# Performance work log

Hardware: AMD Instinct MI355X
Metric: run time of the kernel (lower is better)

Reference implementation:

```python
import jax, jax.numpy as jnp
import numpy as np

E, DIM, HID, OUT = 8, 128, 512, 128
B, HH, WW = 16, 64, 64
N = HH * WW
EPS = 1e-6


def setup_inputs() -> dict:
    key = jax.random.key(0)
    ks = jax.random.split(key, 8)
    return {
        "x": jax.random.normal(ks[0], (B, N, DIM), jnp.float32),
        "H": HH,
        "W": WW,
        "wg": jax.random.normal(ks[1], (DIM, E), jnp.float32) * 0.02,
        "bg": jnp.zeros((E,), jnp.float32),
        "W1": jax.random.normal(ks[2], (E, DIM, HID), jnp.float32) * 0.02,
        "B1": jnp.zeros((E, HID), jnp.float32),
        "Wd": jax.random.normal(ks[3], (E, 3, 3, 1, HID), jnp.float32) * np.sqrt(2.0 / 9.0),
        "Bd": jnp.zeros((E, HID), jnp.float32),
        "W2": jax.random.normal(ks[4], (E, HID, OUT), jnp.float32) * 0.02,
        "B2": jnp.zeros((E, OUT), jnp.float32),
    }


def reference(x, H, W, wg, bg, W1, B1, Wd, Bd, W2, B2):
    Bb, Nn, C = x.shape
    e = wg.shape[1]
    hid = W1.shape[2]

    # ---- SwitchGate (faithful to original, including the dim-1 scatter) ----
    gate_scores = jax.nn.softmax(x @ wg + bg, axis=-1)  # (B,N,E)
    capacity = float(int(1.0 * Bb))  # capacity_factor = 1.0
    top1 = jnp.argmax(gate_scores, axis=-1)  # (B,N)
    # torch: zeros_like(gs).scatter_(1, idx, 1) -> mask[b, idx[b,n,0], 0] = 1
    mask = jnp.zeros_like(gate_scores).at[jnp.arange(Bb)[:, None], top1, 0].set(1.0)
    masked = gate_scores * mask
    denom = masked.sum(axis=0, keepdims=True) + EPS
    gate_scores = masked / denom * capacity
    gate_scores = jnp.nan_to_num(gate_scores)

    # ---- all-experts MixFFN (fc1 -> dwconv -> gelu -> fc2) ----
    h = jnp.einsum('bnd,edh->ebnh', x, W1) + B1[:, None, None, :]  # (E,B,N,hid)
    h = h.reshape(e, Bb, H, W, hid)  # NHWC per expert

    def expert_dwconv(hi, k, bb):
        y = jax.lax.conv_general_dilated(
            hi, k, window_strides=(1, 1), padding='SAME',
            dimension_numbers=('NHWC', 'HWIO', 'NHWC'),
            feature_group_count=hid)
        return y + bb

    h = jax.vmap(expert_dwconv)(h, Wd, Bd)  # (E,B,H,W,hid)
    h = jax.nn.gelu(h.reshape(e, Bb, Nn, hid), approximate=False)
    expert_out = jnp.einsum('ebnh,eho->ebno', h, W2) + B2[:, None, None, :]  # (E,B,N,O)
    expert_out = jnp.nan_to_num(expert_out)

    # weighted combine: sum_e gate[b,n,e] * expert_out[e,b,n,:]
    moe_output = jnp.einsum('bne,ebno->bno', gate_scores, expert_out)
    return moe_output
```

## Files before the change

kernel.cpp:

```cpp
#include <hip/hip_runtime.h>
#include <math.h>

#define NB   16
#define NTOK 4096
#define DIM  128
#define NE   8
#define HID  512
#define NOUT 128
#define GBLK 512


__global__ __launch_bounds__(256) void gate_kernel(
    const float4* __restrict__ x,
    const float* __restrict__ wg,
    const float* __restrict__ bg,
    float* __restrict__ s0,
    unsigned char* __restrict__ hitpart,
    float4* __restrict__ out)
{
    __shared__ float4 lw4[NE][DIM / 4];
    __shared__ float lbg[NE];
    __shared__ unsigned int lmask;

    int tid = threadIdx.x;
    {
        int e = tid >> 5, s = tid & 31, d0 = s * 4;
        float4 w;
        w.x = wg[(d0 + 0) * NE + e];
        w.y = wg[(d0 + 1) * NE + e];
        w.z = wg[(d0 + 2) * NE + e];
        w.w = wg[(d0 + 3) * NE + e];
        lw4[e][s] = w;
    }
    if (tid < NE) lbg[tid] = bg[tid];
    if (tid == 0) lmask = 0u;
    __syncthreads();

    int sub  = tid & 7;
    int tgrp = tid >> 3;

    float4 wv[NE][4];
    #pragma unroll
    for (int e = 0; e < NE; e++)
        #pragma unroll
        for (int k = 0; k < 4; k++) wv[e][k] = lw4[e][sub + 8 * k];

    #pragma unroll 2
    for (int it = 0; it < 4; it++) {
        int tok = (blockIdx.x << 7) + (it << 5) + tgrp;
        int b   = tok >> 12;
        int n   = tok & 4095;
        size_t base = (size_t)tok * 32 + sub;

        float4 zz = make_float4(0.f, 0.f, 0.f, 0.f);
        out[base]      = zz;
        out[base + 8]  = zz;
        out[base + 16] = zz;
        out[base + 24] = zz;

        float4 xv0 = x[base];
        float4 xv1 = x[base + 8];
        float4 xv2 = x[base + 16];
        float4 xv3 = x[base + 24];

        float z[NE];
        #pragma unroll
        for (int e = 0; e < NE; e++) {
            z[e] = xv0.x * wv[e][0].x + xv0.y * wv[e][0].y
                 + xv0.z * wv[e][0].z + xv0.w * wv[e][0].w
                 + xv1.x * wv[e][1].x + xv1.y * wv[e][1].y
                 + xv1.z * wv[e][1].z + xv1.w * wv[e][1].w
                 + xv2.x * wv[e][2].x + xv2.y * wv[e][2].y
                 + xv2.z * wv[e][2].z + xv2.w * wv[e][2].w
                 + xv3.x * wv[e][3].x + xv3.y * wv[e][3].y
                 + xv3.z * wv[e][3].z + xv3.w * wv[e][3].w;
        }

        #pragma unroll
        for (int off = 1; off <= 4; off <<= 1) {
            #pragma unroll
            for (int e = 0; e < NE; e++) z[e] += __shfl_xor(z[e], off);
        }

        if (sub == 0) {
            float zf[NE];
            #pragma unroll
            for (int e = 0; e < NE; e++) zf[e] = z[e] + lbg[e];

            int am = 0;
            float mz = zf[0];
            #pragma unroll
            for (int e = 1; e < NE; e++) {
                if (zf[e] > mz) { mz = zf[e]; am = e; }
            }
            atomicOr(&lmask, 1u << am);

            if (n < 8) {
                float s = 0.f;
                #pragma unroll
                for (int e = 0; e < NE; e++) s += expf(zf[e] - mz);
                s0[b * NE + n] = expf(zf[0] - mz) / s;
            }
        }
    }

    __syncthreads();
    if (tid == 0) hitpart[blockIdx.x] = (unsigned char)lmask;
}

__global__ __launch_bounds__(256) void expert_kernel(
    const float* __restrict__ x,
    const float* __restrict__ W1,
    const float* __restrict__ B1,
    const float* __restrict__ Wd,
    const float* __restrict__ Bd,
    const float* __restrict__ W2,
    const float* __restrict__ B2,
    const float* __restrict__ s0,
    const unsigned char* __restrict__ hitpart,
    float* __restrict__ out)
{
    __shared__ float4 xs4[6][32];
    __shared__ float4 redb[128][6];
    __shared__ float gls[HID];
    __shared__ float red2[256];
    __shared__ unsigned int hm[NB];
    __shared__ float gate_s;

    int b = blockIdx.x >> 3;
    int w = blockIdx.x & 7;
    int tid = threadIdx.x;

    if (tid < NB) {
        const uint4* hp = (const uint4*)hitpart;
        uint4 v0 = hp[tid * 2], v1 = hp[tid * 2 + 1];
        unsigned int m = v0.x | v0.y | v0.z | v0.w | v1.x | v1.y | v1.z | v1.w;
        m |= m >> 16; m |= m >> 8; m &= 0xffu;
        hm[tid] = m;
    }

    if (tid < 192) {
        int p = tid >> 5, dq = tid & 31;
        int row = p / 3, ci = p % 3;
        int col = w - 1 + ci;
        if (col < 0) col = 0;
        xs4[p][dq] = ((const float4*)x)[((size_t)b * NTOK + row * 64 + col) * 32 + dq];
    }
    __syncthreads();

    if (tid == 0) {
        float denom = 1e-6f, mine = 0.f;
        for (int bb = 0; bb < NB; bb++) {
            float v = ((hm[bb] >> w) & 1u) ? s0[bb * NE + w] : 0.f;
            denom += v;
            if (bb == b) mine = v;
        }
        gate_s = 16.0f * mine / denom;
    }

    int q  = tid & 127;
    int kh = tid >> 7;
    float4 acc[6];
    #pragma unroll
    for (int p = 0; p < 6; p++) acc[p] = make_float4(0.f, 0.f, 0.f, 0.f);

    const float4* W14 = (const float4*)W1;
    #pragma unroll 4
    for (int s = 0; s < 16; s++) {
        int d0 = kh * 64 + s * 4;
        float4 wv0 = W14[(size_t)(d0 + 0) * 128 + q];
        float4 wv1 = W14[(size_t)(d0 + 1) * 128 + q];
        float4 wv2 = W14[(size_t)(d0 + 2) * 128 + q];
        float4 wv3 = W14[(size_t)(d0 + 3) * 128 + q];
        #pragma unroll
        for (int p = 0; p < 6; p++) {
            float4 xv = xs4[p][kh * 16 + s];
            acc[p].x += xv.x * wv0.x + xv.y * wv1.x + xv.z * wv2.x + xv.w * wv3.x;
            acc[p].y += xv.x * wv0.y + xv.y * wv1.y + xv.z * wv2.y + xv.w * wv3.y;
            acc[p].z += xv.x * wv0.z + xv.y * wv1.z + xv.z * wv2.z + xv.w * wv3.z;
            acc[p].w += xv.x * wv0.w + xv.y * wv1.w + xv.z * wv2.w + xv.w * wv3.w;
        }
    }

    if (kh == 1) {
        #pragma unroll
        for (int p = 0; p < 6; p++) redb[q][p] = acc[p];
    }
    __syncthreads();

    if (kh == 0) {
        #pragma unroll
        for (int p = 0; p < 6; p++) {
            float4 r = redb[q][p];
            acc[p].x += r.x; acc[p].y += r.y; acc[p].z += r.z; acc[p].w += r.w;
        }
        float4 b1 = ((const float4*)B1)[q];
        float4 y  = ((const float4*)Bd)[q];
        #pragma unroll
        for (int ci = 0; ci < 3; ci++) {
            int col = w - 1 + ci;
            if (col < 0) continue;
            float4 wda = ((const float4*)Wd)[(3 + ci) * 128 + q];
            float4 wdb = ((const float4*)Wd)[(6 + ci) * 128 + q];
            float4 a0 = acc[ci];
            float4 a1 = acc[3 + ci];
            y.x += (a0.x + b1.x) * wda.x + (a1.x + b1.x) * wdb.x;
            y.y += (a0.y + b1.y) * wda.y + (a1.y + b1.y) * wdb.y;
            y.z += (a0.z + b1.z) * wda.z + (a1.z + b1.z) * wdb.z;
            y.w += (a0.w + b1.w) * wda.w + (a1.w + b1.w) * wdb.w;
        }
        const float k = 0.70710678118654752f;
        float4 g;
        g.x = 0.5f * y.x * (1.0f + erff(y.x * k));
        g.y = 0.5f * y.y * (1.0f + erff(y.y * k));
        g.z = 0.5f * y.z * (1.0f + erff(y.z * k));
        g.w = 0.5f * y.w * (1.0f + erff(y.w * k));
        ((float4*)gls)[q] = g;
    }
    __syncthreads();

    int o    = tid & 127;
    int half = tid >> 7;
    const float* wp = W2 + (size_t)(half * 256) * NOUT + o;
    const float4* gp = (const float4*)&gls[half * 256];
    float a = 0.f;
    #pragma unroll
    for (int cb = 0; cb < 256; cb += 32) {
        float wv[32];
        #pragma unroll
        for (int k2 = 0; k2 < 32; k2++) wv[k2] = wp[(size_t)(cb + k2) * NOUT];
        #pragma unroll
        for (int k2 = 0; k2 < 32; k2 += 4) {
            float4 g = gp[(cb + k2) >> 2];
            a += g.x * wv[k2] + g.y * wv[k2 + 1] + g.z * wv[k2 + 2] + g.w * wv[k2 + 3];
        }
    }
    red2[tid] = a;
    __syncthreads();
    if (tid < 128) {
        out[((size_t)b * NTOK + w) * NOUT + o] =
            (red2[tid] + red2[tid + 128] + B2[o]) * gate_s;
    }
}

extern "C" void kernel_launch(void* const* d_in, const int* in_sizes, int n_in,
                              void* d_out, int out_size, void* d_ws, size_t ws_size,
                              hipStream_t stream) {
    const float* x  = (const float*)d_in[0];
    const float* wg = (const float*)d_in[3];
    const float* bg = (const float*)d_in[4];
    const float* W1 = (const float*)d_in[5];
    const float* B1 = (const float*)d_in[6];
    const float* Wd = (const float*)d_in[7];
    const float* Bd = (const float*)d_in[8];
    const float* W2 = (const float*)d_in[9];
    const float* B2 = (const float*)d_in[10];

    float* s0              = (float*)d_ws;
    unsigned char* hitpart = (unsigned char*)d_ws + 512;

    gate_kernel<<<GBLK, 256, 0, stream>>>(
        (const float4*)x, wg, bg, s0, hitpart, (float4*)d_out);
    expert_kernel<<<NB * 8, 256, 0, stream>>>(
        x, W1, B1, Wd, Bd, W2, B2, s0, hitpart, (float*)d_out);
}
```

Before: 121.9 us.

## Fuse gate and expert kernels into one launch with global-counter sync

Merges the gating kernel and the expert kernel into a single launch. The expert blocks come first in the grid so their MLP work overlaps with the gate blocks. Before writing output, each expert block spin-waits on a global counter until all gate blocks have published their hit masks and softmax values, and a second counter resets state for the next call. It also uses nontemporal loads and stores for x and the zero-fill, and skips zeroing rows the expert blocks overwrite. This removes a kernel launch boundary, but it relies on gate blocks making progress while expert blocks spin, and that forward progress is not guaranteed.

```diff
diff --git a/kernel.cpp b/kernel.cpp
--- a/kernel.cpp
+++ b/kernel.cpp
@@ -1,143 +1,149 @@
 #include <hip/hip_runtime.h>
 #include <math.h>
 
-#define NB   16
-#define NTOK 4096
-#define DIM  128
-#define NE   8
-#define HID  512
-#define NOUT 128
-#define GBLK 512
-
-
-__global__ __launch_bounds__(256) void gate_kernel(
-    const float4* __restrict__ x,
+#define NB    16
+#define NTOK  4096
+#define DIM   128
+#define NE    8
+#define HID   512
+#define NOUT  128
+#define NEXP  128
+#define NGATE 512
+
+typedef float f4 __attribute__((ext_vector_type(4)));
+
+__device__ unsigned int g_hit[NGATE];
+__device__ float        g_s0[NB * NE];
+__device__ int          g_cnt1 = 0;
+__device__ int          g_cnt2 = 0;
+
+__global__ __launch_bounds__(256) void moe_fused(
+    const float* __restrict__ x,
     const float* __restrict__ wg,
     const float* __restrict__ bg,
-    float* __restrict__ s0,
-    unsigned char* __restrict__ hitpart,
-    float4* __restrict__ out)
-{
-    __shared__ float4 lw4[NE][DIM / 4];
-    __shared__ float lbg[NE];
-    __shared__ unsigned int lmask;
-
-    int tid = threadIdx.x;
-    {
-        int e = tid >> 5, s = tid & 31, d0 = s * 4;
-        float4 w;
-        w.x = wg[(d0 + 0) * NE + e];
-        w.y = wg[(d0 + 1) * NE + e];
-        w.z = wg[(d0 + 2) * NE + e];
-        w.w = wg[(d0 + 3) * NE + e];
-        lw4[e][s] = w;
-    }
-    if (tid < NE) lbg[tid] = bg[tid];
-    if (tid == 0) lmask = 0u;
-    __syncthreads();
-
-    int sub  = tid & 7;
-    int tgrp = tid >> 3;
-
-    float4 wv[NE][4];
-    #pragma unroll
-    for (int e = 0; e < NE; e++)
-        #pragma unroll
-        for (int k = 0; k < 4; k++) wv[e][k] = lw4[e][sub + 8 * k];
-
-    #pragma unroll 2
-    for (int it = 0; it < 4; it++) {
-        int tok = (blockIdx.x << 7) + (it << 5) + tgrp;
-        int b   = tok >> 12;
-        int n   = tok & 4095;
-        size_t base = (size_t)tok * 32 + sub;
-
-        float4 zz = make_float4(0.f, 0.f, 0.f, 0.f);
-        out[base]      = zz;
-        out[base + 8]  = zz;
-        out[base + 16] = zz;
-        out[base + 24] = zz;
-
-        float4 xv0 = x[base];
-        float4 xv1 = x[base + 8];
-        float4 xv2 = x[base + 16];
-        float4 xv3 = x[base + 24];
-
-        float z[NE];
-        #pragma unroll
-        for (int e = 0; e < NE; e++) {
-            z[e] = xv0.x * wv[e][0].x + xv0.y * wv[e][0].y
-                 + xv0.z * wv[e][0].z + xv0.w * wv[e][0].w
-                 + xv1.x * wv[e][1].x + xv1.y * wv[e][1].y
-                 + xv1.z * wv[e][1].z + xv1.w * wv[e][1].w
-                 + xv2.x * wv[e][2].x + xv2.y * wv[e][2].y
-                 + xv2.z * wv[e][2].z + xv2.w * wv[e][2].w
-                 + xv3.x * wv[e][3].x + xv3.y * wv[e][3].y
-                 + xv3.z * wv[e][3].z + xv3.w * wv[e][3].w;
-        }
-
-        #pragma unroll
-        for (int off = 1; off <= 4; off <<= 1) {
-            #pragma unroll
-            for (int e = 0; e < NE; e++) z[e] += __shfl_xor(z[e], off);
-        }
-
-        if (sub == 0) {
-            float zf[NE];
-            #pragma unroll
-            for (int e = 0; e < NE; e++) zf[e] = z[e] + lbg[e];
-
-            int am = 0;
-            float mz = zf[0];
-            #pragma unroll
-            for (int e = 1; e < NE; e++) {
-                if (zf[e] > mz) { mz = zf[e]; am = e; }
-            }
-            atomicOr(&lmask, 1u << am);
-
-            if (n < 8) {
-                float s = 0.f;
-                #pragma unroll
-                for (int e = 0; e < NE; e++) s += expf(zf[e] - mz);
-                s0[b * NE + n] = expf(zf[0] - mz) / s;
-            }
-        }
-    }
-
-    __syncthreads();
-    if (tid == 0) hitpart[blockIdx.x] = (unsigned char)lmask;
-}
-
-__global__ __launch_bounds__(256) void expert_kernel(
-    const float* __restrict__ x,
     const float* __restrict__ W1,
     const float* __restrict__ B1,
     const float* __restrict__ Wd,
     const float* __restrict__ Bd,
     const float* __restrict__ W2,
     const float* __restrict__ B2,
-    const float* __restrict__ s0,
-    const unsigned char* __restrict__ hitpart,
-    float* __restrict__ out)
+    float*       __restrict__ out)
 {
+    int tid = threadIdx.x;
+
+    if (blockIdx.x >= NEXP) {
+        int gb = blockIdx.x - NEXP;
+        __shared__ f4 lw4[NE][DIM / 4];
+        __shared__ float lbg[NE];
+        __shared__ unsigned int lmask;
+
+        {
+            int e = tid >> 5, s = tid & 31, d0 = s * 4;
+            f4 w;
+            w.x = wg[(d0 + 0) * NE + e];
+            w.y = wg[(d0 + 1) * NE + e];
+            w.z = wg[(d0 + 2) * NE + e];
+            w.w = wg[(d0 + 3) * NE + e];
+            lw4[e][s] = w;
+        }
+        if (tid < NE) lbg[tid] = bg[tid];
+        if (tid == 0) lmask = 0u;
+        __syncthreads();
+
+        int sub  = tid & 7;
+        int tgrp = tid >> 3;
+
+        f4 wv[NE][4];
+        #pragma unroll
+        for (int e = 0; e < NE; e++)
+            #pragma unroll
+            for (int k = 0; k < 4; k++) wv[e][k] = lw4[e][sub + 8 * k];
+
+        const f4* x4 = (const f4*)x;
+        f4* o4 = (f4*)out;
+
+        #pragma unroll 2
+        for (int it = 0; it < 4; it++) {
+            int tok = (gb << 7) + (it << 5) + tgrp;
+            int b   = tok >> 12;
+            int n   = tok & 4095;
+            size_t base = (size_t)tok * 32 + sub;
+
+            if (n >= 8) {
+                f4 zz = {0.f, 0.f, 0.f, 0.f};
+                __builtin_nontemporal_store(zz, o4 + base);
+                __builtin_nontemporal_store(zz, o4 + base + 8);
+                __builtin_nontemporal_store(zz, o4 + base + 16);
+                __builtin_nontemporal_store(zz, o4 + base + 24);
+            }
+
+            f4 xv0 = __builtin_nontemporal_load(x4 + base);
+            f4 xv1 = __builtin_nontemporal_load(x4 + base + 8);
+            f4 xv2 = __builtin_nontemporal_load(x4 + base + 16);
+            f4 xv3 = __builtin_nontemporal_load(x4 + base + 24);
+
+            float z[NE];
+            #pragma unroll
+            for (int e = 0; e < NE; e++) {
+                z[e] = xv0.x * wv[e][0].x + xv0.y * wv[e][0].y
+                     + xv0.z * wv[e][0].z + xv0.w * wv[e][0].w
+                     + xv1.x * wv[e][1].x + xv1.y * wv[e][1].y
+                     + xv1.z * wv[e][1].z + xv1.w * wv[e][1].w
+                     + xv2.x * wv[e][2].x + xv2.y * wv[e][2].y
+                     + xv2.z * wv[e][2].z + xv2.w * wv[e][2].w
+                     + xv3.x * wv[e][3].x + xv3.y * wv[e][3].y
+                     + xv3.z * wv[e][3].z + xv3.w * wv[e][3].w;
+            }
+
+            #pragma unroll
+            for (int off = 1; off <= 4; off <<= 1) {
+                #pragma unroll
+                for (int e = 0; e < NE; e++) z[e] += __shfl_xor(z[e], off);
+            }
+
+            if (sub == 0) {
+                float zf[NE];
+                #pragma unroll
+                for (int e = 0; e < NE; e++) zf[e] = z[e] + lbg[e];
+
+                int am = 0;
+                float mz = zf[0];
+                #pragma unroll
+                for (int e = 1; e < NE; e++) {
+                    if (zf[e] > mz) { mz = zf[e]; am = e; }
+                }
+                atomicOr(&lmask, 1u << am);
+
+                if (n < 8) {
+                    float ssum = 0.f;
+                    #pragma unroll
+                    for (int e = 0; e < NE; e++) ssum += expf(zf[e] - mz);
+                    __hip_atomic_store(&g_s0[b * NE + n], expf(zf[0] - mz) / ssum,
+                                       __ATOMIC_RELAXED, __HIP_MEMORY_SCOPE_AGENT);
+                }
+            }
+        }
+
+        __syncthreads();
+        if (tid == 0) {
+            __hip_atomic_store(&g_hit[gb], lmask,
+                               __ATOMIC_RELAXED, __HIP_MEMORY_SCOPE_AGENT);
+            __hip_atomic_fetch_add(&g_cnt1, 1,
+                                   __ATOMIC_RELEASE, __HIP_MEMORY_SCOPE_AGENT);
+        }
+        return;
+    }
+
+    int b = blockIdx.x >> 3;
+    int w = blockIdx.x & 7;
+
     __shared__ float4 xs4[6][32];
     __shared__ float4 redb[128][6];
-    __shared__ float gls[HID];
-    __shared__ float red2[256];
-    __shared__ unsigned int hm[NB];
-    __shared__ float gate_s;
-
-    int b = blockIdx.x >> 3;
-    int w = blockIdx.x & 7;
-    int tid = threadIdx.x;
-
-    if (tid < NB) {
-        const uint4* hp = (const uint4*)hitpart;
-        uint4 v0 = hp[tid * 2], v1 = hp[tid * 2 + 1];
-        unsigned int m = v0.x | v0.y | v0.z | v0.w | v1.x | v1.y | v1.z | v1.w;
-        m |= m >> 16; m |= m >> 8; m &= 0xffu;
-        hm[tid] = m;
-    }
+    __shared__ float  gls[HID];
+    __shared__ float  red2[256];
+    __shared__ unsigned int hmred[128];
+    __shared__ float  svred[NB];
+    __shared__ float  gate_s;
 
     if (tid < 192) {
         int p = tid >> 5, dq = tid & 31;
@@ -147,16 +153,6 @@
         xs4[p][dq] = ((const float4*)x)[((size_t)b * NTOK + row * 64 + col) * 32 + dq];
     }
     __syncthreads();
-
-    if (tid == 0) {
-        float denom = 1e-6f, mine = 0.f;
-        for (int bb = 0; bb < NB; bb++) {
-            float v = ((hm[bb] >> w) & 1u) ? s0[bb * NE + w] : 0.f;
-            denom += v;
-            if (bb == b) mine = v;
-        }
-        gate_s = 16.0f * mine / denom;
-    }
 
     int q  = tid & 127;
     int kh = tid >> 7;
@@ -209,12 +205,12 @@
             y.z += (a0.z + b1.z) * wda.z + (a1.z + b1.z) * wdb.z;
             y.w += (a0.w + b1.w) * wda.w + (a1.w + b1.w) * wdb.w;
         }
-        const float k = 0.70710678118654752f;
+        const float kk = 0.70710678118654752f;
         float4 g;
-        g.x = 0.5f * y.x * (1.0f + erff(y.x * k));
-        g.y = 0.5f * y.y * (1.0f + erff(y.y * k));
-        g.z = 0.5f * y.z * (1.0f + erff(y.z * k));
-        g.w = 0.5f * y.w * (1.0f + erff(y.w * k));
+        g.x = 0.5f * y.x * (1.0f + erff(y.x * kk));
+        g.y = 0.5f * y.y * (1.0f + erff(y.y * kk));
+        g.z = 0.5f * y.z * (1.0f + erff(y.z * kk));
+        g.w = 0.5f * y.w * (1.0f + erff(y.w * kk));
         ((float4*)gls)[q] = g;
     }
     __syncthreads();
@@ -226,20 +222,68 @@
     float a = 0.f;
     #pragma unroll
     for (int cb = 0; cb < 256; cb += 32) {
-        float wv[32];
-        #pragma unroll
-        for (int k2 = 0; k2 < 32; k2++) wv[k2] = wp[(size_t)(cb + k2) * NOUT];
+        float wvv[32];
+        #pragma unroll
+        for (int k2 = 0; k2 < 32; k2++) wvv[k2] = wp[(size_t)(cb + k2) * NOUT];
         #pragma unroll
         for (int k2 = 0; k2 < 32; k2 += 4) {
             float4 g = gp[(cb + k2) >> 2];
-            a += g.x * wv[k2] + g.y * wv[k2 + 1] + g.z * wv[k2 + 2] + g.w * wv[k2 + 3];
+            a += g.x * wvv[k2] + g.y * wvv[k2 + 1] + g.z * wvv[k2 + 2] + g.w * wvv[k2 + 3];
         }
     }
     red2[tid] = a;
     __syncthreads();
+
+    if (tid == 0) {
+        while (__hip_atomic_load(&g_cnt1, __ATOMIC_RELAXED,
+                                 __HIP_MEMORY_SCOPE_AGENT) < NGATE)
+            __builtin_amdgcn_s_sleep(8);
+        (void)__hip_atomic_load(&g_cnt1, __ATOMIC_ACQUIRE,
+                                __HIP_MEMORY_SCOPE_AGENT);
+    }
+    __syncthreads();
+
+    if (tid < 128) {
+        unsigned int m = 0;
+        #pragma unroll
+        for (int i = 0; i < 4; i++)
+            m |= __hip_atomic_load(&g_hit[tid * 4 + i], __ATOMIC_RELAXED,
+                                   __HIP_MEMORY_SCOPE_AGENT);
+        hmred[tid] = m;
+    }
+    __syncthreads();
+    if (tid < NB) {
+        unsigned int m = 0;
+        #pragma unroll
+        for (int i = 0; i < 8; i++) m |= hmred[tid * 8 + i];
+        float v = 0.f;
+        if ((m >> w) & 1u)
+            v = __hip_atomic_load(&g_s0[tid * NE + w], __ATOMIC_RELAXED,
+                                  __HIP_MEMORY_SCOPE_AGENT);
+        svred[tid] = v;
+    }
+    __syncthreads();
+    if (tid == 0) {
+        float denom = 1e-6f;
+        #pragma unroll
+        for (int bb = 0; bb < NB; bb++) denom += svred[bb];
+        gate_s = 16.0f * svred[b] / denom;
+    }
+    __syncthreads();
+
     if (tid < 128) {
         out[((size_t)b * NTOK + w) * NOUT + o] =
             (red2[tid] + red2[tid + 128] + B2[o]) * gate_s;
+    }
+
+    __syncthreads();
+    if (tid == 0) {
+        int v = __hip_atomic_fetch_add(&g_cnt2, 1, __ATOMIC_ACQ_REL,
+                                       __HIP_MEMORY_SCOPE_AGENT);
+        if (v == NEXP - 1) {
+            __hip_atomic_store(&g_cnt1, 0, __ATOMIC_RELAXED, __HIP_MEMORY_SCOPE_AGENT);
+            __hip_atomic_store(&g_cnt2, 0, __ATOMIC_RELAXED, __HIP_MEMORY_SCOPE_AGENT);
+        }
     }
 }
 
@@ -255,12 +299,8 @@
     const float* Bd = (const float*)d_in[8];
     const float* W2 = (const float*)d_in[9];
     const float* B2 = (const float*)d_in[10];
-
-    float* s0              = (float*)d_ws;
-    unsigned char* hitpart = (unsigned char*)d_ws + 512;
-
-    gate_kernel<<<GBLK, 256, 0, stream>>>(
-        (const float4*)x, wg, bg, s0, hitpart, (float4*)d_out);
-    expert_kernel<<<NB * 8, 256, 0, stream>>>(
-        x, W1, B1, Wd, Bd, W2, B2, s0, hitpart, (float*)d_out);
+    (void)d_ws; (void)ws_size; (void)in_sizes; (void)n_in; (void)out_size;
+
+    moe_fused<<<NEXP + NGATE, 256, 0, stream>>>(
+        x, wg, bg, W1, B1, Wd, Bd, W2, B2, (float*)d_out);
 }
```

Result: slower. 137.6 us (+12.9%).
